# Kernel tuning notes

Measured on AMD Instinct MI355X. Metric: run time of the kernel, lower is better.

## Reference

```python
import jax, jax.numpy as jnp
import numpy as np

D = 768      # num_hiddens (hardcoded by dense1/dense2/ln in the source)
H = 12       # num_heads
NEG = -1000000.0
EPS = 1e-5


def setup_inputs() -> dict:
    key = jax.random.key(0)
    ks = jax.random.split(key, 14)
    B, Lq, Lk = 8, 1024, 1024
    s = 0.02
    return {
        "queries": jax.random.normal(ks[0], (B, Lq, D), dtype=jnp.float32),
        "keys":    jax.random.normal(ks[1], (B, Lk, D), dtype=jnp.float32),
        "values":  jax.random.normal(ks[2], (B, Lk, D), dtype=jnp.float32),
        # binary padding masks; count_nonzero along axis 1 gives valid lens
        "mask_1": jax.random.randint(ks[3], (B, Lk), 0, 2, dtype=jnp.int32),
        "mask_2": jax.random.randint(ks[4], (B, Lq), 0, 2, dtype=jnp.int32),
        # projection weights stored as [in, out] (torch Linear is y = x @ W.T)
        "Wq": jax.random.normal(ks[5], (D, D), dtype=jnp.float32) * s,
        "Wk": jax.random.normal(ks[6], (D, D), dtype=jnp.float32) * s,
        "Wv": jax.random.normal(ks[7], (D, D), dtype=jnp.float32) * s,
        "Wo": jax.random.normal(ks[8], (D, D), dtype=jnp.float32) * s,
        "d1_w": jax.random.normal(ks[9], (D, D), dtype=jnp.float32) * s,
        "d1_b": jnp.zeros((D,), dtype=jnp.float32),
        "d2_w": jax.random.normal(ks[10], (D, D), dtype=jnp.float32) * s,
        "d2_b": jnp.zeros((D,), dtype=jnp.float32),
        "ln_g": jnp.ones((D,), dtype=jnp.float32),
        "ln_b": jnp.zeros((D,), dtype=jnp.float32),
    }


def _cross_att(queries, keys, values, mask_1, mask_2,
               Wq, Wk, Wv, Wo, d1_w, d1_b, d2_w, d2_b, ln_g, ln_b):
    B, Lq, _ = queries.shape
    Lk = keys.shape[1]
    hd = D // H
    # project + split heads: [B, H, L, hd]
    q = (queries @ Wq).reshape(B, Lq, H, hd).transpose(0, 2, 1, 3)
    k = (keys    @ Wk).reshape(B, Lk, H, hd).transpose(0, 2, 1, 3)
    v = (values  @ Wv).reshape(B, Lk, H, hd).transpose(0, 2, 1, 3)
    scores = jnp.einsum('bhqd,bhkd->bhqk', q, k) / jnp.sqrt(jnp.float32(hd))
    # dual-axis prefix mask from nonzero counts
    vl1 = jnp.sum(mask_1 != 0, axis=1)  # [B], masks key axis
    vl2 = jnp.sum(mask_2 != 0, axis=1)  # [B], masks query axis
    col_ok = jnp.arange(Lk)[None, None, None, :] < vl1[:, None, None, None]
    row_ok = jnp.arange(Lq)[None, None, :, None] < vl2[:, None, None, None]
    scores = jnp.where(col_ok & row_ok, scores, NEG)
    attn = jax.nn.softmax(scores, axis=-1)
    out = jnp.einsum('bhqk,bhkd->bhqd', attn, v)
    out = out.transpose(0, 2, 1, 3).reshape(B, Lq, D)
    mha = out @ Wo
    ffn = jax.nn.relu(mha @ d1_w + d1_b) @ d2_w + d2_b
    x = ffn + mha  # dropout is identity in eval
    mu = jnp.mean(x, axis=-1, keepdims=True)
    var = jnp.mean(jnp.square(x - mu), axis=-1, keepdims=True)
    return (x - mu) / jnp.sqrt(var + EPS) * ln_g + ln_b


def reference(queries, keys, values, mask_1, mask_2,
              Wq, Wk, Wv, Wo, d1_w, d1_b, d2_w, d2_b, ln_g, ln_b):
    return _cross_att(queries, keys, values, mask_1, mask_2,
                      Wq, Wk, Wv, Wo, d1_w, d1_b, d2_w, d2_b, ln_g, ln_b)
```

## Files before the change

### kernel.cpp

```cpp
#include <hip/hip_runtime.h>
#include <hip/hip_bf16.h>
#include <type_traits>

#define DM   768
#define NH   12
#define HD   64
#define BATCH 8
#define SEQ  1024
#define NROWS (BATCH * SEQ)

typedef short bf16x8 __attribute__((ext_vector_type(8)));
typedef float f32x4 __attribute__((ext_vector_type(4)));

__device__ inline unsigned short f2b(float x) {
    union { float f; unsigned int u; } v; v.f = x;
    return (unsigned short)((v.u + 0x8000u) >> 16);
}
__device__ inline unsigned int f2b2(float lo, float hi) {
    union { float f; unsigned int u; } a, b; a.f = lo; b.f = hi;
    return __builtin_amdgcn_perm(b.u + 0x8000u, a.u + 0x8000u, 0x07060302u);
}
__device__ inline float b2f(unsigned short u) {
    union { float f; unsigned int x; } v; v.x = ((unsigned int)u) << 16;
    return v.f;
}

__device__ inline void gld16(const unsigned short* g, unsigned short* l) {
    __builtin_amdgcn_global_load_lds(
        (const __attribute__((address_space(1))) unsigned int*)g,
        (__attribute__((address_space(3))) unsigned int*)l, 16, 0, 0);
}

__device__ __forceinline__ void mm_loop(const unsigned short* __restrict__ A,
                                        const unsigned short* __restrict__ Wt,
                                        int m0, int n0, int t,
                                        unsigned short (*As)[128][32],
                                        unsigned short (*Ws)[128][32],
                                        f32x4 (&acc)[4][4]) {
    const int w = t >> 6, lane = t & 63;
    const int quad = lane >> 4, l16 = lane & 15;
    const int wm = w & 1, wn = w >> 1;
    const int srow = 16 * w + (lane >> 2);
    const int scol = 8 * ((lane & 3) ^ ((lane >> 3) & 3));
    const int swr = (quad ^ ((l16 >> 1) & 3)) * 8;

#pragma unroll
    for (int i = 0; i < 4; ++i)
#pragma unroll
        for (int j = 0; j < 4; ++j) acc[i][j] = (f32x4){0.f, 0.f, 0.f, 0.f};

    const unsigned short* aP = &A[(size_t)(m0 + srow) * DM + scol];
    const unsigned short* wP = &Wt[(size_t)(n0 + srow) * DM + scol];

    auto stage = [&](int kk, int b) {
#pragma unroll
        for (int j = 0; j < 2; ++j) {
            gld16(aP + (size_t)(64 * j) * DM + kk * 32, &As[b][16 * w + 64 * j][0]);
            gld16(wP + (size_t)(64 * j) * DM + kk * 32, &Ws[b][16 * w + 64 * j][0]);
        }
    };
    auto compute = [&](int b) {
        bf16x8 av[4], bv[4];
#pragma unroll
        for (int i = 0; i < 4; ++i)
            av[i] = *(const bf16x8*)&As[b][wm * 64 + 16 * i + l16][swr];
#pragma unroll
        for (int i = 0; i < 4; ++i)
            bv[i] = *(const bf16x8*)&Ws[b][wn * 64 + 16 * i + l16][swr];
#pragma unroll
        for (int i = 0; i < 4; ++i)
#pragma unroll
            for (int j = 0; j < 4; ++j)
                acc[i][j] = __builtin_amdgcn_mfma_f32_16x16x32_bf16(bv[j], av[i], acc[i][j], 0, 0, 0);
    };

    stage(0, 0);
    stage(1, 1);
    int b = 0;
#pragma unroll 1
    for (int k = 0; k < 22; ++k) {
        int nb = b + 2; if (nb >= 3) nb -= 3;
        stage(k + 2, nb);
        asm volatile("s_waitcnt vmcnt(8)" ::: "memory");
        __builtin_amdgcn_s_barrier();
        compute(b);
        asm volatile("" ::: "memory");
        __builtin_amdgcn_s_barrier();
        if (++b == 3) b = 0;
    }
    asm volatile("s_waitcnt vmcnt(4)" ::: "memory");
    __builtin_amdgcn_s_barrier();
    compute(b);
    asm volatile("" ::: "memory");
    __builtin_amdgcn_s_barrier();
    if (++b == 3) b = 0;
    asm volatile("s_waitcnt vmcnt(0)" ::: "memory");
    __builtin_amdgcn_s_barrier();
    compute(b);
}

__global__ __launch_bounds__(256) void prep_kernel(const float* __restrict__ w0,
                                                   const float* __restrict__ w1,
                                                   const float* __restrict__ w2,
                                                   const float* __restrict__ w3,
                                                   const float* __restrict__ w4,
                                                   const float* __restrict__ w5,
                                                   unsigned short* __restrict__ wt,
                                                   unsigned short* __restrict__ wob,
                                                   const float* __restrict__ qin,
                                                   const float* __restrict__ kin,
                                                   const float* __restrict__ vin,
                                                   unsigned short* __restrict__ oq,
                                                   unsigned short* __restrict__ ok,
                                                   unsigned short* __restrict__ ov) {
    const int z = blockIdx.z;
    const int t = threadIdx.x;

    if (z >= 6) {
        const int linear = (z - 6) * 576 + blockIdx.y * 24 + blockIdx.x;
        const int c0 = linear * 2;
        const int g = c0 / 3072;
        const int r = c0 % 3072;
        const float* src = (g == 0) ? qin : (g == 1) ? kin : vin;
        unsigned short* dst = (g == 0) ? oq : (g == 1) ? ok : ov;
        const size_t i = ((size_t)r * 256 + t) * 8;
        float4 f0 = ((const float4*)(src + i))[0];
        float4 f1 = ((const float4*)(src + i))[1];
        float4 f2 = ((const float4*)(src + i + 2048))[0];
        float4 f3 = ((const float4*)(src + i + 2048))[1];
        uint4 p;
        p.x = f2b2(f0.x, f0.y); p.y = f2b2(f0.z, f0.w);
        p.z = f2b2(f1.x, f1.y); p.w = f2b2(f1.z, f1.w);
        *(uint4*)(dst + i) = p;
        p.x = f2b2(f2.x, f2.y); p.y = f2b2(f2.z, f2.w);
        p.z = f2b2(f3.x, f3.y); p.w = f2b2(f3.z, f3.w);
        *(uint4*)(dst + i + 2048) = p;
        return;
    }

    {
        __shared__ float tile[32][33];
        const float* W = (z == 0) ? w0 : (z == 1) ? w1 : (z == 2) ? w2
                       : (z == 3) ? w3 : (z == 4) ? w4 : w5;
        unsigned short* Wt = wt + (size_t)z * DM * DM;
        const int n0 = blockIdx.x * 32;
        const int k0 = blockIdx.y * 32;
        const int tx = t & 31;
        const int ty = t >> 5;
        float v[4];
#pragma unroll
        for (int r = 0; r < 4; ++r) {
            v[r] = W[(size_t)(k0 + ty + 8 * r) * DM + n0 + tx];
            tile[ty + 8 * r][tx] = v[r];
        }
        if (z == 3) {
#pragma unroll
            for (int r = 0; r < 4; ++r)
                wob[(size_t)(k0 + ty + 8 * r) * DM + n0 + tx] = f2b(v[r]);
        }
        __syncthreads();
#pragma unroll
        for (int r = 0; r < 4; ++r)
            Wt[(size_t)(n0 + ty + 8 * r) * DM + k0 + tx] = f2b(tile[tx][ty + 8 * r]);
    }
}

__global__ __launch_bounds__(256) void qkv_gemm(const unsigned short* __restrict__ aq,
                                                const unsigned short* __restrict__ akk,
                                                const unsigned short* __restrict__ av_,
                                                unsigned short* __restrict__ wt,
                                                const unsigned short* __restrict__ wob,
                                                unsigned short* __restrict__ c0,
                                                unsigned short* __restrict__ c1,
                                                unsigned short* __restrict__ c2,
                                                const int* __restrict__ m1,
                                                const int* __restrict__ m2,
                                                int* __restrict__ lens) {
    __shared__ __align__(16) unsigned short As[3][128][32];
    __shared__ __align__(16) unsigned short Ws[3][128][32];

    const int t = threadIdx.x;
    const size_t WT = (size_t)DM * DM;

    const unsigned short* A;
    const unsigned short* Wop;
    unsigned short* C;
    float cs;
    int m0, n0;

    if (blockIdx.y == 0) {
        if (blockIdx.x >= 52) return;
        if (blockIdx.x >= 36) {
            const int bid = blockIdx.x - 36;
            int* redi = (int*)&As[0][0][0];
            const int b = bid & 7;
            const int* m = (bid < 8) ? m1 : m2;
            int cnt = 0;
            for (int i = t; i < SEQ; i += 256) cnt += (m[b * SEQ + i] != 0) ? 1 : 0;
            redi[t] = cnt;
            __syncthreads();
            for (int off = 128; off > 0; off >>= 1) {
                if (t < off) redi[t] += redi[t + off];
                __syncthreads();
            }
            if (t == 0) lens[bid] = redi[0];
            return;
        }
        A = wt + 4 * WT;
        Wop = wob;
        C = wt + 6 * WT;
        cs = 1.0f;
        m0 = (blockIdx.x % 6) * 128;
        n0 = (blockIdx.x / 6) * 128;
    } else {
        const int yy = blockIdx.y - 1;
        const int g = yy / 6;
        m0 = blockIdx.x * 128;
        n0 = (yy % 6) * 128;
        A = (g == 0) ? aq : (g == 1) ? akk : av_;
        Wop = wt + (size_t)g * WT;
        C = (g == 0) ? c0 : (g == 1) ? c1 : c2;
        cs = (g == 0) ? 0.18033688f : 1.0f;
    }

    f32x4 acc[4][4];
    mm_loop(A, Wop, m0, n0, t, As, Ws, acc);

    const int w = t >> 6, lane = t & 63;
    const int quad = lane >> 4, l16 = lane & 15;
    const int wm = w & 1, wn = w >> 1;

#pragma unroll
    for (int i = 0; i < 4; ++i) {
        const int tok = m0 + wm * 64 + 16 * i + l16;
        unsigned short* crow = &C[(size_t)tok * DM + n0 + wn * 64 + quad * 4];
#pragma unroll
        for (int j = 0; j < 4; ++j) {
            uint2 pr;
            pr.x = f2b2(acc[i][j][0] * cs, acc[i][j][1] * cs);
            pr.y = f2b2(acc[i][j][2] * cs, acc[i][j][3] * cs);
            *(uint2*)(crow + 16 * j) = pr;
        }
    }
}

__global__ __launch_bounds__(256) void vpart_kernel(const unsigned short* __restrict__ v,
                                                    float* __restrict__ vp) {
    __shared__ float red[4][64];
    const int t = threadIdx.x;
    const int bh = blockIdx.x;
    const int chunk = blockIdx.y;
    const int b = bh / NH, h = bh % NH;
    const int d = t & 63, rg = t >> 6;
    const unsigned short* base =
        v + (size_t)(b * SEQ + chunk * 128 + rg * 32) * DM + h * HD + d;
    float s = 0.0f;
#pragma unroll 4
    for (int i = 0; i < 32; ++i) s += b2f(base[(size_t)i * DM]);
    red[rg][d] = s;
    __syncthreads();
    if (rg == 0)
        vp[((size_t)bh * 8 + chunk) * 64 + d] = red[0][d] + red[1][d] + red[2][d] + red[3][d];
}

template <typename CT>
__global__ __launch_bounds__(256) void gemm_bf(const unsigned short* __restrict__ A,
                                               const unsigned short* __restrict__ Wt,
                                               CT* __restrict__ C,
                                               const float* __restrict__ bias,
                                               const unsigned short* __restrict__ res,
                                               int relu) {
    __shared__ __align__(16) unsigned short As[3][128][32];
    __shared__ __align__(16) unsigned short Ws[3][128][32];

    const int t = threadIdx.x;
    const int m0 = blockIdx.x * 128;
    const int n0 = blockIdx.y * 128;

    f32x4 acc[4][4];
    mm_loop(A, Wt, m0, n0, t, As, Ws, acc);

    const int w = t >> 6, lane = t & 63;
    const int quad = lane >> 4, l16 = lane & 15;
    const int wm = w & 1, wn = w >> 1;

#pragma unroll
    for (int i = 0; i < 4; ++i) {
        const int tok = m0 + wm * 64 + 16 * i + l16;
#pragma unroll
        for (int j = 0; j < 4; ++j) {
            const int fb = n0 + wn * 64 + 16 * j + quad * 4;
            float cv0 = acc[i][j][0], cv1 = acc[i][j][1];
            float cv2 = acc[i][j][2], cv3 = acc[i][j][3];
            if (bias) {
                const float4 bb = *(const float4*)&bias[fb];
                cv0 += bb.x; cv1 += bb.y; cv2 += bb.z; cv3 += bb.w;
            }
            if (relu) {
                cv0 = fmaxf(cv0, 0.0f); cv1 = fmaxf(cv1, 0.0f);
                cv2 = fmaxf(cv2, 0.0f); cv3 = fmaxf(cv3, 0.0f);
            }
            if (res) {
                const uint2 rr = *(const uint2*)&res[(size_t)tok * DM + fb];
                cv0 += b2f((unsigned short)(rr.x & 0xffffu));
                cv1 += b2f((unsigned short)(rr.x >> 16));
                cv2 += b2f((unsigned short)(rr.y & 0xffffu));
                cv3 += b2f((unsigned short)(rr.y >> 16));
            }
            if constexpr (std::is_same<CT, float>::value) {
                float4 o4; o4.x = cv0; o4.y = cv1; o4.z = cv2; o4.w = cv3;
                *(float4*)&C[(size_t)tok * DM + fb] = o4;
            } else {
                uint2 pr;
                pr.x = f2b2(cv0, cv1);
                pr.y = f2b2(cv2, cv3);
                *(uint2*)&C[(size_t)tok * DM + fb] = pr;
            }
        }
    }
}

__global__ __launch_bounds__(256) void gemm_mh(const unsigned short* __restrict__ A,
                                               const unsigned short* __restrict__ wt,
                                               unsigned short* __restrict__ cm,
                                               unsigned short* __restrict__ ch,
                                               const float* __restrict__ d1b) {
    __shared__ __align__(16) unsigned short As[3][128][32];
    __shared__ __align__(16) unsigned short Ws[3][128][32];

    const int t = threadIdx.x;
    const int unit = blockIdx.y / 6;
    const unsigned short* Wt = wt + (size_t)(unit ? 6 : 3) * DM * DM;
    unsigned short* C = unit ? ch : cm;
    const int m0 = blockIdx.x * 128;
    const int n0 = (blockIdx.y % 6) * 128;

    f32x4 acc[4][4];
    mm_loop(A, Wt, m0, n0, t, As, Ws, acc);

    const int w = t >> 6, lane = t & 63;
    const int quad = lane >> 4, l16 = lane & 15;
    const int wm = w & 1, wn = w >> 1;

#pragma unroll
    for (int i = 0; i < 4; ++i) {
        const int tok = m0 + wm * 64 + 16 * i + l16;
#pragma unroll
        for (int j = 0; j < 4; ++j) {
            const int fb = n0 + wn * 64 + 16 * j + quad * 4;
            float cv0 = acc[i][j][0], cv1 = acc[i][j][1];
            float cv2 = acc[i][j][2], cv3 = acc[i][j][3];
            if (unit) {
                const float4 bb = *(const float4*)&d1b[fb];
                cv0 = fmaxf(cv0 + bb.x, 0.0f);
                cv1 = fmaxf(cv1 + bb.y, 0.0f);
                cv2 = fmaxf(cv2 + bb.z, 0.0f);
                cv3 = fmaxf(cv3 + bb.w, 0.0f);
            }
            uint2 pr;
            pr.x = f2b2(cv0, cv1);
            pr.y = f2b2(cv2, cv3);
            *(uint2*)&C[(size_t)tok * DM + fb] = pr;
        }
    }
}

__global__ __launch_bounds__(256) void attn_mfma(const unsigned short* Q,
                                                 const unsigned short* __restrict__ K,
                                                 const unsigned short* __restrict__ V,
                                                 unsigned short* O,
                                                 const int* __restrict__ lens,
                                                 const float* __restrict__ vp) {
    __shared__ __align__(16) unsigned short Ks[64][72];
    __shared__ __align__(16) unsigned short Vt[64][72];
    __shared__ __align__(16) unsigned short Ps[4][16][72];

    const int t = threadIdx.x;
    const int bid = blockIdx.x;
    const int q0 = (bid & 15) * 64;
    const int h = (bid >> 4) % NH;
    const int b = bid / (16 * NH);
    const int vl1 = lens[b];
    const int vl2 = lens[8 + b];
    const int wid = t >> 6;
    const int lane = t & 63;
    const int quad = lane >> 4;
    const int l16 = lane & 15;
    const size_t vpb = (size_t)(b * NH + h) * 8 * 64;

    if (q0 >= vl2 || vl1 == 0) {
        float vm[4];
#pragma unroll
        for (int ct = 0; ct < 4; ++ct) {
            float s = 0.0f;
#pragma unroll
            for (int c = 0; c < 8; ++c) s += vp[vpb + (size_t)c * 64 + 16 * ct + l16];
            vm[ct] = s * (1.0f / 1024.0f);
        }
#pragma unroll
        for (int r = 0; r < 4; ++r) {
            const size_t row = (size_t)(b * SEQ + q0 + 16 * wid + quad * 4 + r);
#pragma unroll
            for (int ct = 0; ct < 4; ++ct)
                O[row * DM + h * HD + 16 * ct + l16] = f2b(vm[ct]);
        }
        return;
    }

    bf16x8 qa0, qa1;
    {
        const unsigned short* qp =
            &Q[(size_t)(b * SEQ + q0 + 16 * wid + l16) * DM + h * HD + quad * 8];
        qa0 = *(const bf16x8*)qp;
        qa1 = *(const bf16x8*)(qp + 32);
    }

    f32x4 o[4];
#pragma unroll
    for (int ct = 0; ct < 4; ++ct) o[ct] = (f32x4){0.f, 0.f, 0.f, 0.f};
    float suml[4];
    bool rbad[4];
#pragma unroll
    for (int r = 0; r < 4; ++r) {
        suml[r] = 0.0f;
        rbad[r] = (q0 + 16 * wid + quad * 4 + r) >= vl2;
    }

    const int nt = (vl1 + 63) >> 6;

    const int kkr = t >> 3;
    const int khc = (t & 7) * 8;
    const unsigned short* kbase = &K[(size_t)(b * SEQ) * DM + h * HD];
    const unsigned short* vbase = &V[(size_t)(b * SEQ) * DM + h * HD];

    uint4 kr0 = *(const uint4*)&kbase[(size_t)kkr * DM + khc];
    uint4 kr1 = *(const uint4*)&kbase[(size_t)(kkr + 32) * DM + khc];
    uint4 vr0 = *(const uint4*)&vbase[(size_t)lane * DM + wid * 16];
    uint4 vr1 = *(const uint4*)&vbase[(size_t)lane * DM + wid * 16 + 8];

    const int k2 = l16 >> 2;

    for (int tile = 0; tile < nt; ++tile) {
        const int c0 = tile * 64;
        *(uint4*)&Ks[kkr][khc] = kr0;
        *(uint4*)&Ks[kkr + 32][khc] = kr1;
        {
            union { uint4 u; unsigned short s[8]; } va, vb;
            va.u = vr0; vb.u = vr1;
#pragma unroll
            for (int j = 0; j < 8; ++j) Vt[wid * 16 + j][lane] = va.s[j];
#pragma unroll
            for (int j = 0; j < 8; ++j) Vt[wid * 16 + 8 + j][lane] = vb.s[j];
        }
        __syncthreads();

        if (tile < nt - 1) {
            const int c1 = c0 + 64;
            kr0 = *(const uint4*)&kbase[(size_t)(c1 + kkr) * DM + khc];
            kr1 = *(const uint4*)&kbase[(size_t)(c1 + kkr + 32) * DM + khc];
            vr0 = *(const uint4*)&vbase[(size_t)(c1 + lane) * DM + wid * 16];
            vr1 = *(const uint4*)&vbase[(size_t)(c1 + lane) * DM + wid * 16 + 8];
        }

        f32x4 s[4];
#pragma unroll
        for (int ct = 0; ct < 4; ++ct) {
            f32x4 acc = (f32x4){0.f, 0.f, 0.f, 0.f};
            bf16x8 b0v = *(const bf16x8*)&Ks[16 * ct + l16][quad * 8];
            bf16x8 b1v = *(const bf16x8*)&Ks[16 * ct + l16][32 + quad * 8];
            acc = __builtin_amdgcn_mfma_f32_16x16x32_bf16(qa0, b0v, acc, 0, 0, 0);
            acc = __builtin_amdgcn_mfma_f32_16x16x32_bf16(qa1, b1v, acc, 0, 0, 0);
            s[ct] = acc;
        }
#pragma unroll
        for (int ct = 0; ct < 4; ++ct) {
            const bool kok = (c0 + 16 * ct + l16) < vl1;
#pragma unroll
            for (int r = 0; r < 4; ++r) {
                float e = __builtin_amdgcn_exp2f(s[ct][r]);
                float p = kok ? e : 0.0f;
                s[ct][r] = p;
                suml[r] += p;
            }
        }
#pragma unroll
        for (int ct = 0; ct < 4; ++ct) {
            const int gidx = 2 * ct + (l16 >> 3);
            const int c = l16 & 7;
            const int gs = (gidx ^ quad) * 8 + c;
#pragma unroll
            for (int r = 0; r < 4; ++r)
                Ps[wid][quad * 4 + r][gs] = f2b(s[ct][r]);
        }
        bf16x8 pa0 = *(const bf16x8*)&Ps[wid][l16][(quad ^ k2) * 8];
        bf16x8 pa1 = *(const bf16x8*)&Ps[wid][l16][((4 + quad) ^ k2) * 8];
#pragma unroll
        for (int ct = 0; ct < 4; ++ct) {
            bf16x8 vb0 = *(const bf16x8*)&Vt[16 * ct + l16][quad * 8];
            bf16x8 vb1 = *(const bf16x8*)&Vt[16 * ct + l16][32 + quad * 8];
            o[ct] = __builtin_amdgcn_mfma_f32_16x16x32_bf16(pa0, vb0, o[ct], 0, 0, 0);
            o[ct] = __builtin_amdgcn_mfma_f32_16x16x32_bf16(pa1, vb1, o[ct], 0, 0, 0);
        }
        __syncthreads();
    }

#pragma unroll
    for (int d = 1; d < 16; d <<= 1) {
#pragma unroll
        for (int r = 0; r < 4; ++r) suml[r] += __shfl_xor(suml[r], d, 64);
    }

    float vm[4];
    if (rbad[0] || rbad[3]) {
#pragma unroll
        for (int ct = 0; ct < 4; ++ct) {
            float s = 0.0f;
#pragma unroll
            for (int c = 0; c < 8; ++c) s += vp[vpb + (size_t)c * 64 + 16 * ct + l16];
            vm[ct] = s * (1.0f / 1024.0f);
        }
    }
#pragma unroll
    for (int r = 0; r < 4; ++r) {
        const float inv = 1.0f / suml[r];
        const size_t row = (size_t)(b * SEQ + q0 + 16 * wid + quad * 4 + r);
#pragma unroll
        for (int ct = 0; ct < 4; ++ct) {
            const float val = rbad[r] ? vm[ct] : o[ct][r] * inv;
            O[row * DM + h * HD + 16 * ct + l16] = f2b(val);
        }
    }
}

__global__ __launch_bounds__(256) void ln_kernel(float* __restrict__ X,
                                                 const float* __restrict__ g,
                                                 const float* __restrict__ bvec) {
    __shared__ float red[256];
    const int row = blockIdx.x;
    const int t = threadIdx.x;
    float* xr = X + (size_t)row * DM;
    float x0 = xr[t];
    float x1 = xr[t + 256];
    float x2 = xr[t + 512];
    red[t] = x0 + x1 + x2;
    __syncthreads();
    for (int off = 128; off > 0; off >>= 1) {
        if (t < off) red[t] += red[t + off];
        __syncthreads();
    }
    float mu = red[0] * (1.0f / 768.0f);
    __syncthreads();
    float d0 = x0 - mu, d1 = x1 - mu, d2 = x2 - mu;
    red[t] = d0 * d0 + d1 * d1 + d2 * d2;
    __syncthreads();
    for (int off = 128; off > 0; off >>= 1) {
        if (t < off) red[t] += red[t + off];
        __syncthreads();
    }
    float rstd = rsqrtf(red[0] * (1.0f / 768.0f) + 1e-5f);
    xr[t]       = d0 * rstd * g[t]       + bvec[t];
    xr[t + 256] = d1 * rstd * g[t + 256] + bvec[t + 256];
    xr[t + 512] = d2 * rstd * g[t + 512] + bvec[t + 512];
}

extern "C" void kernel_launch(void* const* d_in, const int* in_sizes, int n_in,
                              void* d_out, int out_size, void* d_ws, size_t ws_size,
                              hipStream_t stream) {
    const float* queries = (const float*)d_in[0];
    const float* keys    = (const float*)d_in[1];
    const float* values  = (const float*)d_in[2];
    const int* mask1 = (const int*)d_in[3];
    const int* mask2 = (const int*)d_in[4];
    const float* Wq  = (const float*)d_in[5];
    const float* Wk  = (const float*)d_in[6];
    const float* Wv  = (const float*)d_in[7];
    const float* Wo  = (const float*)d_in[8];
    const float* d1w = (const float*)d_in[9];
    const float* d1b = (const float*)d_in[10];
    const float* d2w = (const float*)d_in[11];
    const float* d2b = (const float*)d_in[12];
    const float* lng = (const float*)d_in[13];
    const float* lnb = (const float*)d_in[14];

    char* ws = (char*)d_ws;
    int* lens = (int*)ws;
    float* vp = (float*)(ws + 256);
    const size_t VP = (size_t)96 * 8 * 64 * sizeof(float);
    const size_t NB = (size_t)NROWS * DM * sizeof(unsigned short);
    const size_t WT = (size_t)DM * DM;
    unsigned short* b0 = (unsigned short*)(ws + 256 + VP);
    unsigned short* b1 = (unsigned short*)(ws + 256 + VP + NB);
    unsigned short* b2 = (unsigned short*)(ws + 256 + VP + 2 * NB);
    unsigned short* wt = (unsigned short*)(ws + 256 + VP + 3 * NB);
    unsigned short* aq = (unsigned short*)(ws + 256 + VP + 3 * NB + 7 * WT * sizeof(unsigned short));
    unsigned short* ak = aq + (size_t)NROWS * DM;
    unsigned short* av = ak + (size_t)NROWS * DM;
    unsigned short* wob = av + (size_t)NROWS * DM;
    float* xout = (float*)d_out;

    prep_kernel<<<dim3(24, 24, 14), 256, 0, stream>>>(Wq, Wk, Wv, Wo, d1w, d2w,
                                                      wt, wob, queries, keys, values,
                                                      aq, ak, av);

    qkv_gemm<<<dim3(64, 19), 256, 0, stream>>>(aq, ak, av, wt, wob, b0, b1, b2,
                                               mask1, mask2, lens);

    vpart_kernel<<<dim3(96, 8), 256, 0, stream>>>(b2, vp);

    attn_mfma<<<16 * NH * BATCH, 256, 0, stream>>>(b0, b1, b2, b0, lens, vp);

    gemm_mh<<<dim3(64, 12), 256, 0, stream>>>(b0, wt, b1, b2, d1b);

    gemm_bf<float><<<dim3(64, 6), 256, 0, stream>>>(b2, wt + 5 * WT, xout, d2b, b1, 0);

    ln_kernel<<<NROWS, 256, 0, stream>>>(xout, lng, lnb);
}
```

Measured before the change: 311.6 us.

## Replace triple-buffered GEMM pipeline with double buffering and widen conversion blocks

Replaces the shared GEMM mainloop's three-stage LDS ring, which used explicit vmcnt waits and split barriers, with a simpler two-buffer loop that prefetches the next K-slice and ends each step with one __syncthreads. This lowers LDS use per block, which may let more blocks fit on a CU, but the full barrier drains the prefetch every iteration so load latency is hidden less. Separately, the input fp32-to-bf16 conversion blocks each handle four chunks instead of two, cutting that part of the prep grid from 8 z-slices to 4. Also moves the cs=1.0 default into its declaration.

```diff
diff --git a/kernel.cpp b/kernel.cpp
--- a/kernel.cpp
+++ b/kernel.cpp
@@ -31,12 +31,12 @@
         (__attribute__((address_space(3))) unsigned int*)l, 16, 0, 0);
 }
 
-__device__ __forceinline__ void mm_loop(const unsigned short* __restrict__ A,
-                                        const unsigned short* __restrict__ Wt,
-                                        int m0, int n0, int t,
-                                        unsigned short (*As)[128][32],
-                                        unsigned short (*Ws)[128][32],
-                                        f32x4 (&acc)[4][4]) {
+__device__ __forceinline__ void mm2(const unsigned short* __restrict__ A,
+                                    const unsigned short* __restrict__ Wt,
+                                    int m0, int n0, int t,
+                                    unsigned short (*As)[128][32],
+                                    unsigned short (*Ws)[128][32],
+                                    f32x4 (&acc)[4][4]) {
     const int w = t >> 6, lane = t & 63;
     const int quad = lane >> 4, l16 = lane & 15;
     const int wm = w & 1, wn = w >> 1;
@@ -49,54 +49,38 @@
 #pragma unroll
         for (int j = 0; j < 4; ++j) acc[i][j] = (f32x4){0.f, 0.f, 0.f, 0.f};
 
-    const unsigned short* aP = &A[(size_t)(m0 + srow) * DM + scol];
-    const unsigned short* wP = &Wt[(size_t)(n0 + srow) * DM + scol];
-
-    auto stage = [&](int kk, int b) {
-#pragma unroll
-        for (int j = 0; j < 2; ++j) {
-            gld16(aP + (size_t)(64 * j) * DM + kk * 32, &As[b][16 * w + 64 * j][0]);
-            gld16(wP + (size_t)(64 * j) * DM + kk * 32, &Ws[b][16 * w + 64 * j][0]);
-        }
-    };
-    auto compute = [&](int b) {
+#pragma unroll
+    for (int j = 0; j < 2; ++j) {
+        gld16(&A[(size_t)(m0 + srow + 64 * j) * DM + scol], &As[0][16 * w + 64 * j][0]);
+        gld16(&Wt[(size_t)(n0 + srow + 64 * j) * DM + scol], &Ws[0][16 * w + 64 * j][0]);
+    }
+    __syncthreads();
+
+    for (int k0 = 0; k0 < DM; k0 += 32) {
+        const int cur = (k0 >> 5) & 1;
+        if (k0 + 32 < DM) {
+#pragma unroll
+            for (int j = 0; j < 2; ++j) {
+                gld16(&A[(size_t)(m0 + srow + 64 * j) * DM + k0 + 32 + scol],
+                      &As[cur ^ 1][16 * w + 64 * j][0]);
+                gld16(&Wt[(size_t)(n0 + srow + 64 * j) * DM + k0 + 32 + scol],
+                      &Ws[cur ^ 1][16 * w + 64 * j][0]);
+            }
+        }
         bf16x8 av[4], bv[4];
 #pragma unroll
         for (int i = 0; i < 4; ++i)
-            av[i] = *(const bf16x8*)&As[b][wm * 64 + 16 * i + l16][swr];
+            av[i] = *(const bf16x8*)&As[cur][wm * 64 + 16 * i + l16][swr];
 #pragma unroll
         for (int i = 0; i < 4; ++i)
-            bv[i] = *(const bf16x8*)&Ws[b][wn * 64 + 16 * i + l16][swr];
+            bv[i] = *(const bf16x8*)&Ws[cur][wn * 64 + 16 * i + l16][swr];
 #pragma unroll
         for (int i = 0; i < 4; ++i)
 #pragma unroll
             for (int j = 0; j < 4; ++j)
                 acc[i][j] = __builtin_amdgcn_mfma_f32_16x16x32_bf16(bv[j], av[i], acc[i][j], 0, 0, 0);
-    };
-
-    stage(0, 0);
-    stage(1, 1);
-    int b = 0;
-#pragma unroll 1
-    for (int k = 0; k < 22; ++k) {
-        int nb = b + 2; if (nb >= 3) nb -= 3;
-        stage(k + 2, nb);
-        asm volatile("s_waitcnt vmcnt(8)" ::: "memory");
-        __builtin_amdgcn_s_barrier();
-        compute(b);
-        asm volatile("" ::: "memory");
-        __builtin_amdgcn_s_barrier();
-        if (++b == 3) b = 0;
-    }
-    asm volatile("s_waitcnt vmcnt(4)" ::: "memory");
-    __builtin_amdgcn_s_barrier();
-    compute(b);
-    asm volatile("" ::: "memory");
-    __builtin_amdgcn_s_barrier();
-    if (++b == 3) b = 0;
-    asm volatile("s_waitcnt vmcnt(0)" ::: "memory");
-    __builtin_amdgcn_s_barrier();
-    compute(b);
+        __syncthreads();
+    }
 }
 
 __global__ __launch_bounds__(256) void prep_kernel(const float* __restrict__ w0,
@@ -118,23 +102,27 @@
 
     if (z >= 6) {
         const int linear = (z - 6) * 576 + blockIdx.y * 24 + blockIdx.x;
-        const int c0 = linear * 2;
+        const int c0 = linear * 4;
         const int g = c0 / 3072;
         const int r = c0 % 3072;
         const float* src = (g == 0) ? qin : (g == 1) ? kin : vin;
         unsigned short* dst = (g == 0) ? oq : (g == 1) ? ok : ov;
         const size_t i = ((size_t)r * 256 + t) * 8;
-        float4 f0 = ((const float4*)(src + i))[0];
-        float4 f1 = ((const float4*)(src + i))[1];
-        float4 f2 = ((const float4*)(src + i + 2048))[0];
-        float4 f3 = ((const float4*)(src + i + 2048))[1];
-        uint4 p;
-        p.x = f2b2(f0.x, f0.y); p.y = f2b2(f0.z, f0.w);
-        p.z = f2b2(f1.x, f1.y); p.w = f2b2(f1.z, f1.w);
-        *(uint4*)(dst + i) = p;
-        p.x = f2b2(f2.x, f2.y); p.y = f2b2(f2.z, f2.w);
-        p.z = f2b2(f3.x, f3.y); p.w = f2b2(f3.z, f3.w);
-        *(uint4*)(dst + i + 2048) = p;
+        float4 f[8];
+#pragma unroll
+        for (int c = 0; c < 4; ++c) {
+            f[2 * c]     = ((const float4*)(src + i + (size_t)c * 2048))[0];
+            f[2 * c + 1] = ((const float4*)(src + i + (size_t)c * 2048))[1];
+        }
+#pragma unroll
+        for (int c = 0; c < 4; ++c) {
+            uint4 p;
+            p.x = f2b2(f[2 * c].x, f[2 * c].y);
+            p.y = f2b2(f[2 * c].z, f[2 * c].w);
+            p.z = f2b2(f[2 * c + 1].x, f[2 * c + 1].y);
+            p.w = f2b2(f[2 * c + 1].z, f[2 * c + 1].w);
+            *(uint4*)(dst + i + (size_t)c * 2048) = p;
+        }
         return;
     }
 
@@ -176,8 +164,8 @@
                                                 const int* __restrict__ m1,
                                                 const int* __restrict__ m2,
                                                 int* __restrict__ lens) {
-    __shared__ __align__(16) unsigned short As[3][128][32];
-    __shared__ __align__(16) unsigned short Ws[3][128][32];
+    __shared__ __align__(16) unsigned short As[2][128][32];
+    __shared__ __align__(16) unsigned short Ws[2][128][32];
 
     const int t = threadIdx.x;
     const size_t WT = (size_t)DM * DM;
@@ -185,7 +173,7 @@
     const unsigned short* A;
     const unsigned short* Wop;
     unsigned short* C;
-    float cs;
+    float cs = 1.0f;
     int m0, n0;
 
     if (blockIdx.y == 0) {
@@ -209,7 +197,6 @@
         A = wt + 4 * WT;
         Wop = wob;
         C = wt + 6 * WT;
-        cs = 1.0f;
         m0 = (blockIdx.x % 6) * 128;
         n0 = (blockIdx.x / 6) * 128;
     } else {
@@ -224,7 +211,7 @@
     }
 
     f32x4 acc[4][4];
-    mm_loop(A, Wop, m0, n0, t, As, Ws, acc);
+    mm2(A, Wop, m0, n0, t, As, Ws, acc);
 
     const int w = t >> 6, lane = t & 63;
     const int quad = lane >> 4, l16 = lane & 15;
@@ -270,15 +257,15 @@
                                                const float* __restrict__ bias,
                                                const unsigned short* __restrict__ res,
                                                int relu) {
-    __shared__ __align__(16) unsigned short As[3][128][32];
-    __shared__ __align__(16) unsigned short Ws[3][128][32];
+    __shared__ __align__(16) unsigned short As[2][128][32];
+    __shared__ __align__(16) unsigned short Ws[2][128][32];
 
     const int t = threadIdx.x;
     const int m0 = blockIdx.x * 128;
     const int n0 = blockIdx.y * 128;
 
     f32x4 acc[4][4];
-    mm_loop(A, Wt, m0, n0, t, As, Ws, acc);
+    mm2(A, Wt, m0, n0, t, As, Ws, acc);
 
     const int w = t >> 6, lane = t & 63;
     const int quad = lane >> 4, l16 = lane & 15;
@@ -325,8 +312,8 @@
                                                unsigned short* __restrict__ cm,
                                                unsigned short* __restrict__ ch,
                                                const float* __restrict__ d1b) {
-    __shared__ __align__(16) unsigned short As[3][128][32];
-    __shared__ __align__(16) unsigned short Ws[3][128][32];
+    __shared__ __align__(16) unsigned short As[2][128][32];
+    __shared__ __align__(16) unsigned short Ws[2][128][32];
 
     const int t = threadIdx.x;
     const int unit = blockIdx.y / 6;
@@ -336,7 +323,7 @@
     const int n0 = (blockIdx.y % 6) * 128;
 
     f32x4 acc[4][4];
-    mm_loop(A, Wt, m0, n0, t, As, Ws, acc);
+    mm2(A, Wt, m0, n0, t, As, Ws, acc);
 
     const int w = t >> 6, lane = t & 63;
     const int quad = lane >> 4, l16 = lane & 15;
@@ -598,7 +585,7 @@
     unsigned short* wob = av + (size_t)NROWS * DM;
     float* xout = (float*)d_out;
 
-    prep_kernel<<<dim3(24, 24, 14), 256, 0, stream>>>(Wq, Wk, Wv, Wo, d1w, d2w,
+    prep_kernel<<<dim3(24, 24, 10), 256, 0, stream>>>(Wq, Wk, Wv, Wo, d1w, d2w,
                                                       wt, wob, queries, keys, values,
                                                       aq, ak, av);
 
```

Measured after the change: 302.0 us. 3.1% less time.
